# Performance work log

Hardware: AMD Instinct MI355X
Metric: run time of the kernel (lower is better)

Reference implementation:

```python
import jax, jax.numpy as jnp
import numpy as np
from jax import lax

B, T, H, E, V, S = 32, 512, 1024, 300, 32000, 50
NL2 = 4  # 2 layers * 2 directions of encoder hidden


def setup_inputs() -> dict:
    key = jax.random.key(0)
    ks = jax.random.split(key, 20)
    w = 0.05  # small init scale to keep tanh/softmax well-conditioned
    return {
        "enc_out": jax.random.normal(ks[0], (B, T, H), jnp.float32),
        "enc_h": jax.random.normal(ks[1], (NL2, B, H // 2), jnp.float32),
        "enc_c": jax.random.normal(ks[2], (NL2, B, H // 2), jnp.float32),
        "embedding": jax.random.normal(ks[3], (V, E), jnp.float32),
        "attn_W": jax.random.normal(ks[4], (H, 2 * H), jnp.float32) * w,
        "attn_b": jnp.zeros((H,), jnp.float32),
        "v": jax.random.normal(ks[5], (H,), jnp.float32) * w,
        "Wih0": jax.random.normal(ks[6], (4 * H, E + H), jnp.float32) * w,
        "Whh0": jax.random.normal(ks[7], (4 * H, H), jnp.float32) * w,
        "bih0": jnp.zeros((4 * H,), jnp.float32),
        "bhh0": jnp.zeros((4 * H,), jnp.float32),
        "Wih1": jax.random.normal(ks[8], (4 * H, H), jnp.float32) * w,
        "Whh1": jax.random.normal(ks[9], (4 * H, H), jnp.float32) * w,
        "bih1": jnp.zeros((4 * H,), jnp.float32),
        "bhh1": jnp.zeros((4 * H,), jnp.float32),
        "genW": jax.random.normal(ks[10], (V, H), jnp.float32) * w,
        "genb": jnp.zeros((V,), jnp.float32),
        "question": jax.random.randint(ks[11], (B, S), 0, V, jnp.int64),
    }


def _lstm_cell(x, h, c, Wih, Whh, bih, bhh):
    # torch gate order: i, f, g, o
    g = x @ Wih.T + bih + h @ Whh.T + bhh
    i, f, gg, o = jnp.split(g, 4, axis=-1)
    c2 = jax.nn.sigmoid(f) * c + jax.nn.sigmoid(i) * jnp.tanh(gg)
    h2 = jax.nn.sigmoid(o) * jnp.tanh(c2)
    return h2, c2


def reference(enc_out, enc_h, enc_c, embedding, attn_W, attn_b, v,
              Wih0, Whh0, bih0, bhh0, Wih1, Whh1, bih1, bhh1,
              genW, genb, question):
    # merge bidirectional encoder halves: (2L,B,H/2) -> (L,B,H)
    h0 = jnp.concatenate([enc_h[0::2], enc_h[1::2]], axis=2)
    c0 = jnp.concatenate([enc_c[0::2], enc_c[1::2]], axis=2)

    def step(carry, tok):
        h, c = carry  # each (L, B, H)
        emb = embedding[tok]  # (B, E); dropout is identity (eval mode)
        hid = h[-1]  # (B, H), last-layer hidden drives attention
        Hrep = jnp.broadcast_to(hid[:, None, :], enc_out.shape)  # (B,T,H)
        energy = jnp.tanh(jnp.concatenate([Hrep, enc_out], axis=-1) @ attn_W.T + attn_b)
        scores = jnp.einsum('bth,h->bt', energy, v)
        aw = jax.nn.softmax(scores, axis=1)  # (B, T)
        ctx = jnp.einsum('bt,bth->bh', aw, enc_out)  # (B, H)
        x = jnp.concatenate([emb, ctx], axis=-1)  # (B, E+H)
        h0n, c0n = _lstm_cell(x, h[0], c[0], Wih0, Whh0, bih0, bhh0)
        h1n, c1n = _lstm_cell(h0n, h[1], c[1], Wih1, Whh1, bih1, bhh1)
        out = jax.nn.log_softmax(h1n @ genW.T + genb, axis=-1)  # (B, V)
        return (jnp.stack([h0n, h1n]), jnp.stack([c0n, c1n])), out

    _, outs = lax.scan(step, (h0, c0), question.T)  # outs: (S, B, V)
    return jnp.transpose(outs, (1, 0, 2))  # (B, S, V)
```

## Files before the change

kernel.cpp:

```cpp
#include <hip/hip_runtime.h>
#include <hip/hip_bf16.h>
#include <math.h>

#define DEVI static __device__ __forceinline__

namespace {
constexpr int B = 32, T = 512, H = 1024, E = 300, V = 32000, S = 50;
constexpr int KX = E + H;
constexpr int K0 = 2368;
constexpr int K1 = 2048;
constexpr int MG = V + H;
}

typedef __bf16 bf16x8 __attribute__((ext_vector_type(8)));
typedef float f32x4 __attribute__((ext_vector_type(4)));

DEVI float bf2f(unsigned short u) { union { unsigned int i; float f; } v; v.i = (unsigned int)u << 16; return v.f; }
DEVI unsigned short f2bf(float f) {
  union { float f; unsigned int i; } v; v.f = f;
  unsigned int x = v.i;
  return (unsigned short)((x + 0x7fffu + ((x >> 16) & 1u)) >> 16);
}
DEVI unsigned char f2e4m3(float x) {
  union { float f; unsigned int u; } v;
  v.f = x;
  unsigned int s = (v.u >> 24) & 0x80u;
  v.u &= 0x7FFFFFFFu;
  if (v.f >= 448.0f) return (unsigned char)(s | 0x7E);
  if (v.f < 0.015625f) {
    int q = (int)rintf(v.f * 512.0f);
    return (unsigned char)(s | (unsigned int)q);
  }
  unsigned int u = v.u;
  unsigned int lsb = (u >> 20) & 1u;
  u += 0x0007FFFFu + lsb;
  unsigned int exp = (u >> 23) - 120u;
  unsigned int man = (u >> 20) & 7u;
  return (unsigned char)(s | (exp << 3) | man);
}
DEVI float e4m3f(unsigned int u) {
  unsigned int bits = ((u & 0x80u) << 24) | ((u & 0x7Fu) << 20);
  union { unsigned int i; float f; } v; v.i = bits;
  return v.f * 0x1p120f;
}
#if __has_builtin(__builtin_amdgcn_rcpf)
DEVI float frcp(float x) { return __builtin_amdgcn_rcpf(x); }
#else
DEVI float frcp(float x) { return 1.0f / x; }
#endif
DEVI float sigm(float x) { return frcp(1.0f + __expf(-x)); }
DEVI float tanh_(float x) { return 1.0f - 2.0f * frcp(__expf(2.0f * x) + 1.0f); }

__global__ __launch_bounds__(256) void k_cast_gen(const float* __restrict__ genW,
    const float* __restrict__ attn_W, unsigned char* __restrict__ Wbig8) {
  size_t i4 = ((size_t)blockIdx.x * 256 + threadIdx.x) * 4;
  if (i4 >= (size_t)MG * H) return;
  int row = (int)(i4 >> 10), k = (int)(i4 & 1023);
  const float* src = row < V ? &genW[((size_t)row << 10) + k]
                             : &attn_W[(size_t)(row - V) * (2 * H) + k];
  float4 v = *(const float4*)src;
  uchar4 o; o.x = f2e4m3(v.x); o.y = f2e4m3(v.y); o.z = f2e4m3(v.z); o.w = f2e4m3(v.w);
  *(uchar4*)&Wbig8[i4] = o;
}

__global__ __launch_bounds__(256) void k_cast_l0(const float* __restrict__ Wih,
    const float* __restrict__ Whh, unsigned short* __restrict__ Wc) {
  int m = blockIdx.x;
  int g = m & 3, n = m >> 2, srow = g * H + n;
  for (int i = threadIdx.x; i < K0 / 4; i += 256) {
    int k = i * 4;
    float4 v;
    if (k < KX) v = *(const float4*)&Wih[(size_t)srow * KX + k];
    else if (k < KX + H) v = *(const float4*)&Whh[(size_t)srow * H + (k - KX)];
    else v = make_float4(0.f, 0.f, 0.f, 0.f);
    ushort4 o; o.x = f2bf(v.x); o.y = f2bf(v.y); o.z = f2bf(v.z); o.w = f2bf(v.w);
    *(ushort4*)&Wc[(size_t)m * K0 + k] = o;
  }
}

__global__ __launch_bounds__(256) void k_cast_l1(const float* __restrict__ Wih,
    const float* __restrict__ Whh, unsigned short* __restrict__ Wc) {
  int m = blockIdx.x;
  int g = m & 3, n = m >> 2, srow = g * H + n;
  for (int i = threadIdx.x; i < K1 / 4; i += 256) {
    int k = i * 4;
    float4 v = (k < H) ? *(const float4*)&Wih[(size_t)srow * H + k]
                       : *(const float4*)&Whh[(size_t)srow * H + (k - H)];
    ushort4 o; o.x = f2bf(v.x); o.y = f2bf(v.y); o.z = f2bf(v.z); o.w = f2bf(v.w);
    *(ushort4*)&Wc[(size_t)m * K1 + k] = o;
  }
}

__global__ __launch_bounds__(256) void k_cast_attnr(const float* __restrict__ attn_W,
                                                    unsigned short* __restrict__ Wr) {
  size_t i4 = ((size_t)blockIdx.x * 256 + threadIdx.x) * 4;
  if (i4 >= (size_t)H * H) return;
  int n = (int)(i4 >> 10), k = (int)(i4 & 1023);
  float4 v = *(const float4*)&attn_W[(size_t)n * (2 * H) + H + k];
  ushort4 o; o.x = f2bf(v.x); o.y = f2bf(v.y); o.z = f2bf(v.z); o.w = f2bf(v.w);
  *(ushort4*)&Wr[i4] = o;
}

__global__ void k_bias(const float* bih0, const float* bhh0,
                       const float* bih1, const float* bhh1,
                       float* bc0, float* bc1) {
  int idx = blockIdx.x * 256 + threadIdx.x;
  if (idx < 4096) { int g = idx & 3, n = idx >> 2; bc0[idx] = bih0[g * H + n] + bhh0[g * H + n]; }
  else if (idx < 8192) { int m = idx - 4096; int g = m & 3, n = m >> 2; bc1[m] = bih1[g * H + n] + bhh1[g * H + n]; }
}

__global__ __launch_bounds__(256) void k_cast_enc(const float* __restrict__ src,
    unsigned short* __restrict__ dst, unsigned char* __restrict__ dst8) {
  size_t i4 = ((size_t)blockIdx.x * 256 + threadIdx.x) * 4;
  if (i4 >= (size_t)B * T * H) return;
  float4 v = *(const float4*)&src[i4];
  ushort4 o; o.x = f2bf(v.x); o.y = f2bf(v.y); o.z = f2bf(v.z); o.w = f2bf(v.w);
  *(ushort4*)&dst[i4] = o;
  uchar4 o8; o8.x = f2e4m3(v.x); o8.y = f2e4m3(v.y); o8.z = f2e4m3(v.z); o8.w = f2e4m3(v.w);
  *(uchar4*)&dst8[i4] = o8;
}

__global__ __launch_bounds__(256) void k_init(const float* __restrict__ enc_h,
    const float* __restrict__ enc_c, float* __restrict__ cbuf,
    unsigned short* __restrict__ xc0_0, unsigned short* __restrict__ xc0_1,
    unsigned short* __restrict__ xc1_0, unsigned char* __restrict__ hgen8) {
  int idx = blockIdx.x * 256 + threadIdx.x;
  if (idx < 2 * B * H) {
    int l = idx >> 15, r = idx & 32767, b = r >> 10, hh = r & 1023;
    int half = hh >> 9, hr = hh & 511;
    int src = (2 * l + half) * B * (H / 2) + b * (H / 2) + hr;
    cbuf[idx] = enc_c[src];
    float hv = enc_h[src];
    if (l == 0) xc0_0[(size_t)b * K0 + KX + hh] = f2bf(hv);
    else { xc1_0[(size_t)b * K1 + H + hh] = f2bf(hv); hgen8[(size_t)b * H + hh] = f2e4m3(hv); }
  } else if (idx < 2 * B * H + 2 * B * 20) {
    int j = idx - 2 * B * H;
    int p = j / (B * 20), rr = j % (B * 20), b = rr / 20, kk = rr % 20;
    (p ? xc0_1 : xc0_0)[(size_t)b * K0 + KX + H + kk] = 0;
  }
}

__global__ __launch_bounds__(256) void k_encproj_mfma(const unsigned short* __restrict__ Wr,
    const unsigned short* __restrict__ Xb, const float* __restrict__ attn_b,
    unsigned char* __restrict__ encp8) {
  int wv = threadIdx.x >> 6, lane = threadIdx.x & 63;
  int n0w = blockIdx.x * 64 + wv * 16;
  int m0 = blockIdx.y * 64;
  const unsigned short* Wp = Wr + (size_t)(n0w + (lane & 15)) * H + (lane >> 4) * 8;
  const unsigned short* Xp = Xb + (size_t)(m0 + (lane & 15)) * H + (lane >> 4) * 8;
  f32x4 acc[4] = {{0.f,0.f,0.f,0.f},{0.f,0.f,0.f,0.f},{0.f,0.f,0.f,0.f},{0.f,0.f,0.f,0.f}};
#pragma unroll 2
  for (int k0 = 0; k0 < H; k0 += 32) {
    bf16x8 a = *(const bf16x8*)(Wp + k0);
#pragma unroll
    for (int g = 0; g < 4; g++) {
      bf16x8 b = *(const bf16x8*)(Xp + (size_t)g * 16 * H + k0);
      acc[g] = __builtin_amdgcn_mfma_f32_16x16x32_bf16(a, b, acc[g], 0, 0, 0);
    }
  }
  int nb = n0w + (lane >> 4) * 4;
  f32x4 bi = *(const f32x4*)&attn_b[nb];
#pragma unroll
  for (int g = 0; g < 4; g++) {
    int m = m0 + g * 16 + (lane & 15);
    f32x4 o = acc[g] + bi;
    uchar4 ob; ob.x = f2e4m3(o[0]); ob.y = f2e4m3(o[1]); ob.z = f2e4m3(o[2]); ob.w = f2e4m3(o[3]);
    *(uchar4*)&encp8[(size_t)m * H + nb] = ob;
  }
}

DEVI void gemm_tile_fp8(const unsigned char* __restrict__ W, const unsigned char* __restrict__ X,
                        int m0w, int lane, f32x4& acc0, f32x4& acc1) {
  const unsigned char* Wp = W + (size_t)(m0w + (lane & 15)) * 1024 + (lane >> 4) * 8;
  const unsigned char* Xp = X + (size_t)(lane & 15) * 1024 + (lane >> 4) * 8;
#pragma unroll 4
  for (int k0 = 0; k0 < 1024; k0 += 32) {
    long a  = *(const long*)(Wp + k0);
    long b0 = *(const long*)(Xp + k0);
    long b1 = *(const long*)(Xp + 16 * 1024 + k0);
    acc0 = __builtin_amdgcn_mfma_f32_16x16x32_fp8_fp8(a, b0, acc0, 0, 0, 0);
    acc1 = __builtin_amdgcn_mfma_f32_16x16x32_fp8_fp8(a, b1, acc1, 0, 0, 0);
  }
}

__global__ __launch_bounds__(256, 4) void k_gemm_out_fp8(const unsigned char* __restrict__ W,
    const unsigned char* __restrict__ X, const float* __restrict__ bias, int M0,
    float* __restrict__ out0, int ld0, float* __restrict__ out1, int ld1,
    float* __restrict__ part) {
  __shared__ float esum[4][32];
  int wv = threadIdx.x >> 6, lane = threadIdx.x & 63;
  int m0w = blockIdx.x * 64 + wv * 16;
  f32x4 acc0 = {0.f, 0.f, 0.f, 0.f}, acc1 = acc0;
  gemm_tile_fp8(W, X, m0w, lane, acc0, acc1);
  int r0 = m0w + (lane >> 4) * 4;
  int b = lane & 15;
  float s0 = 0.f, s1 = 0.f;
  if (r0 < M0) {
    f32x4 bi = *(const f32x4*)&bias[r0];
    f32x4 o0 = acc0 + bi, o1 = acc1 + bi;
    *(f32x4*)&out0[(size_t)b * ld0 + r0] = o0;
    *(f32x4*)&out0[(size_t)(b + 16) * ld0 + r0] = o1;
    s0 = __expf(o0[0]) + __expf(o0[1]) + __expf(o0[2]) + __expf(o0[3]);
    s1 = __expf(o1[0]) + __expf(o1[1]) + __expf(o1[2]) + __expf(o1[3]);
  } else {
    int r = r0 - M0;
    *(f32x4*)&out1[(size_t)b * ld1 + r] = acc0;
    *(f32x4*)&out1[(size_t)(b + 16) * ld1 + r] = acc1;
  }
  if (part != nullptr && blockIdx.x < V / 64) {
    s0 += __shfl_xor(s0, 16, 64); s0 += __shfl_xor(s0, 32, 64);
    s1 += __shfl_xor(s1, 16, 64); s1 += __shfl_xor(s1, 32, 64);
    if (lane < 16) { esum[wv][lane] = s0; esum[wv][lane + 16] = s1; }
    __syncthreads();
    if (threadIdx.x < 32)
      part[blockIdx.x * 32 + threadIdx.x] =
          esum[0][threadIdx.x] + esum[1][threadIdx.x] + esum[2][threadIdx.x] + esum[3][threadIdx.x];
  }
}

template <int K>
__global__ __launch_bounds__(512, 2) void k_gemm_lstm(const unsigned short* __restrict__ W,
    const unsigned short* __restrict__ X, const float* __restrict__ bcomb,
    float* __restrict__ c,
    unsigned short* __restrict__ hA, int ldA_, int offA,
    unsigned short* __restrict__ hB, int ldB_, int offB,
    unsigned char* __restrict__ h8) {
  __shared__ f32x4 red[8][64][2];
  int wv = threadIdx.x >> 6, lane = threadIdx.x & 63;
  int m0w = blockIdx.x * 16;
  const unsigned short* Wp = W + (size_t)(m0w + (lane & 15)) * K + (lane >> 4) * 8;
  const unsigned short* Xp = X + (size_t)(lane & 15) * K + (lane >> 4) * 8;
  f32x4 acc0 = {0.f, 0.f, 0.f, 0.f}, acc1 = acc0;
#pragma unroll 2
  for (int k0 = wv * 32; k0 < K; k0 += 256) {
    bf16x8 a  = *(const bf16x8*)(Wp + k0);
    bf16x8 b0 = *(const bf16x8*)(Xp + k0);
    bf16x8 b1 = *(const bf16x8*)(Xp + 16 * K + k0);
    acc0 = __builtin_amdgcn_mfma_f32_16x16x32_bf16(a, b0, acc0, 0, 0, 0);
    acc1 = __builtin_amdgcn_mfma_f32_16x16x32_bf16(a, b1, acc1, 0, 0, 0);
  }
  red[wv][lane][0] = acc0;
  red[wv][lane][1] = acc1;
  __syncthreads();
  if (wv == 0) {
    acc0 = red[0][lane][0] + red[1][lane][0] + red[2][lane][0] + red[3][lane][0]
         + red[4][lane][0] + red[5][lane][0] + red[6][lane][0] + red[7][lane][0];
    acc1 = red[0][lane][1] + red[1][lane][1] + red[2][lane][1] + red[3][lane][1]
         + red[4][lane][1] + red[5][lane][1] + red[6][lane][1] + red[7][lane][1];
    int r0 = m0w + (lane >> 4) * 4;
    int n = r0 >> 2;
    f32x4 bi = *(const f32x4*)&bcomb[r0];
#pragma unroll
    for (int f = 0; f < 2; f++) {
      f32x4 g = f ? acc1 : acc0;
      int b = (lane & 15) + f * 16;
      float gi = g[0] + bi[0], gf = g[1] + bi[1];
      float gg = g[2] + bi[2], go = g[3] + bi[3];
      float cp = c[(size_t)b * H + n];
      float c2 = sigm(gf) * cp + sigm(gi) * tanh_(gg);
      c[(size_t)b * H + n] = c2;
      float h2 = sigm(go) * tanh_(c2);
      unsigned short hb = f2bf(h2);
      hA[(size_t)b * ldA_ + offA + n] = hb;
      if (hB) hB[(size_t)b * ldB_ + offB + n] = hb;
      if (h8) h8[(size_t)b * H + n] = f2e4m3(h2);
    }
  }
}

__global__ __launch_bounds__(256, 4) void k_p1(const unsigned char* __restrict__ encp8,
    const float* __restrict__ hidproj, const float* __restrict__ vvec,
    float* __restrict__ scores,
    const float* __restrict__ logits, const float* __restrict__ part,
    float* __restrict__ out,
    const float* __restrict__ embedding, const int* __restrict__ question,
    unsigned short* __restrict__ xc, int s) {
  int bx = blockIdx.x, tid = threadIdx.x;
  if (bx < 512) {
    int wv = tid >> 6, lane = tid & 63;
    int wid0 = bx * 32 + wv * 8;
    int b = wid0 >> 9;
    const float* hp = hidproj + (size_t)b * H + lane * 16;
    const float* vp = vvec + lane * 16;
    float4 h4[4], v4[4];
#pragma unroll
    for (int i = 0; i < 4; i++) { h4[i] = *(const float4*)&hp[i * 4]; v4[i] = *(const float4*)&vp[i * 4]; }
#pragma unroll
    for (int j = 0; j < 8; j++) {
      const unsigned char* ep = encp8 + (size_t)(wid0 + j) * H + lane * 16;
      uint4 u = *(const uint4*)ep;
      float acc = 0.f;
      unsigned int ws[4] = {u.x, u.y, u.z, u.w};
#pragma unroll
      for (int i = 0; i < 4; i++) {
        unsigned int wd = ws[i];
        acc += v4[i].x * tanh_(e4m3f(wd & 0xFF) + h4[i].x);
        acc += v4[i].y * tanh_(e4m3f((wd >> 8) & 0xFF) + h4[i].y);
        acc += v4[i].z * tanh_(e4m3f((wd >> 16) & 0xFF) + h4[i].z);
        acc += v4[i].w * tanh_(e4m3f(wd >> 24) + h4[i].w);
      }
#pragma unroll
      for (int off = 32; off; off >>= 1) acc += __shfl_xor(acc, off, 64);
      if (lane == 0) scores[wid0 + j] = acc;
    }
  } else if (bx < 768) {
    if (s == 0) return;
    __shared__ float red[256];
    int idx = bx - 512;
    int b = idx >> 3, ch = idx & 7;
    float ssum = 0.f;
    for (int i = tid; i < V / 64; i += 256) ssum += part[i * 32 + b];
    red[tid] = ssum; __syncthreads();
    for (int st = 128; st; st >>= 1) { if (tid < st) red[tid] += red[tid + st]; __syncthreads(); }
    float lse = __logf(red[0]);
    const float* L = logits + (size_t)b * V + ch * 4000;
    float* O = out + ((size_t)b * S + (s - 1)) * V + ch * 4000;
    for (int i = tid; i < 1000; i += 256) {
      float4 v = ((const float4*)L)[i];
      ((float4*)O)[i] = make_float4(v.x - lse, v.y - lse, v.z - lse, v.w - lse);
    }
  } else {
    int b = bx - 768;
    int tok = question[b * S + s];
    for (int e = tid; e < E; e += 256)
      xc[(size_t)b * K0 + e] = f2bf(embedding[(size_t)tok * E + e]);
  }
}

__global__ __launch_bounds__(256, 4) void k_ctx(const float* __restrict__ scores,
    const unsigned char* __restrict__ enc8, unsigned short* __restrict__ xc) {
  int b = blockIdx.x, y = blockIdx.y, tid = threadIdx.x;
  __shared__ float aw[T];
  __shared__ float red[256];
  float s0 = scores[b * T + tid], s1 = scores[b * T + 256 + tid];
  float m = fmaxf(s0, s1);
  red[tid] = m; __syncthreads();
  for (int st = 128; st; st >>= 1) { if (tid < st) red[tid] = fmaxf(red[tid], red[tid + st]); __syncthreads(); }
  m = red[0]; __syncthreads();
  float e0 = __expf(s0 - m), e1 = __expf(s1 - m);
  aw[tid] = e0; aw[tid + 256] = e1;
  red[tid] = e0 + e1; __syncthreads();
  for (int st = 128; st; st >>= 1) { if (tid < st) red[tid] += red[tid + st]; __syncthreads(); }
  float inv = frcp(red[0]);
  __syncthreads();
  int wv = tid >> 6, l = tid & 63;
  int q = l & 7, tp = l >> 3;
  const unsigned char* eb = enc8 + (size_t)b * T * H + y * 64 + q * 8;
  float a[8] = {};
  for (int it = 0; it < 16; it++) {
    int t = it * 32 + wv * 8 + tp;
    uint2 u = *(const uint2*)&eb[(size_t)t * H];
    float w = aw[t];
    a[0] += w * e4m3f(u.x & 0xFF);
    a[1] += w * e4m3f((u.x >> 8) & 0xFF);
    a[2] += w * e4m3f((u.x >> 16) & 0xFF);
    a[3] += w * e4m3f(u.x >> 24);
    a[4] += w * e4m3f(u.y & 0xFF);
    a[5] += w * e4m3f((u.y >> 8) & 0xFF);
    a[6] += w * e4m3f((u.y >> 16) & 0xFF);
    a[7] += w * e4m3f(u.y >> 24);
  }
#pragma unroll
  for (int j = 0; j < 8; j++) {
    a[j] += __shfl_xor(a[j], 8, 64);
    a[j] += __shfl_xor(a[j], 16, 64);
    a[j] += __shfl_xor(a[j], 32, 64);
  }
  __syncthreads();
  if (tp == 0) {
#pragma unroll
    for (int j = 0; j < 8; j++) red[wv * 64 + q * 8 + j] = a[j];
  }
  __syncthreads();
  if (tid < 64) {
    float val = (red[tid] + red[64 + tid] + red[128 + tid] + red[192 + tid]) * inv;
    xc[(size_t)b * K0 + E + y * 64 + tid] = f2bf(val);
  }
}

__global__ __launch_bounds__(256) void k_lsB(const float* __restrict__ logits,
    const float* __restrict__ part, float* __restrict__ out, int s) {
  int b = blockIdx.x, ch = blockIdx.y, tid = threadIdx.x;
  __shared__ float red[256];
  float ssum = 0.f;
  for (int i = tid; i < V / 64; i += 256) ssum += part[i * 32 + b];
  red[tid] = ssum; __syncthreads();
  for (int st = 128; st; st >>= 1) { if (tid < st) red[tid] += red[tid + st]; __syncthreads(); }
  float lse = __logf(red[0]);
  const float* L = logits + (size_t)b * V + ch * 4000;
  float* O = out + ((size_t)b * S + s) * V + ch * 4000;
  for (int i = tid; i < 1000; i += 256) {
    float4 v = ((const float4*)L)[i];
    ((float4*)O)[i] = make_float4(v.x - lse, v.y - lse, v.z - lse, v.w - lse);
  }
}

extern "C" void kernel_launch(void* const* d_in, const int* in_sizes, int n_in,
                              void* d_out, int out_size, void* d_ws, size_t ws_size,
                              hipStream_t stream) {
  const float* enc_out   = (const float*)d_in[0];
  const float* enc_h     = (const float*)d_in[1];
  const float* enc_c     = (const float*)d_in[2];
  const float* embedding = (const float*)d_in[3];
  const float* attn_W    = (const float*)d_in[4];
  const float* attn_b    = (const float*)d_in[5];
  const float* vvec      = (const float*)d_in[6];
  const float* Wih0      = (const float*)d_in[7];
  const float* Whh0      = (const float*)d_in[8];
  const float* bih0      = (const float*)d_in[9];
  const float* bhh0      = (const float*)d_in[10];
  const float* Wih1      = (const float*)d_in[11];
  const float* Whh1      = (const float*)d_in[12];
  const float* bih1      = (const float*)d_in[13];
  const float* bhh1      = (const float*)d_in[14];
  const float* genW      = (const float*)d_in[15];
  const float* genb      = (const float*)d_in[16];
  const int*   question  = (const int*)d_in[17];
  float* out = (float*)d_out;

  char* w = (char*)d_ws;
  auto alloc = [&](size_t bytes) { char* r = w; w += (bytes + 255) & ~(size_t)255; return r; };
  unsigned char*  Wbig8 = (unsigned char*)alloc((size_t)MG * H);
  unsigned short* Wc0   = (unsigned short*)alloc((size_t)4096 * K0 * 2);
  unsigned short* Wc1   = (unsigned short*)alloc((size_t)4096 * K1 * 2);
  unsigned short* encb  = (unsigned short*)alloc((size_t)B * T * H * 2);
  unsigned char*  encb8 = (unsigned char*)alloc((size_t)B * T * H);
  unsigned char*  encp8 = (unsigned char*)alloc((size_t)B * T * H);
  unsigned short* Wr    = (unsigned short*)alloc((size_t)H * H * 2);
  float* bcomb0 = (float*)alloc(4096 * 4);
  float* bcomb1 = (float*)alloc(4096 * 4);
  float* cbuf   = (float*)alloc((size_t)2 * B * H * 4);
  unsigned short* xc0[2] = {(unsigned short*)alloc((size_t)B * K0 * 2),
                            (unsigned short*)alloc((size_t)B * K0 * 2)};
  unsigned short* xc1[2] = {(unsigned short*)alloc((size_t)B * K1 * 2),
                            (unsigned short*)alloc((size_t)B * K1 * 2)};
  unsigned char*  hgen8 = (unsigned char*)alloc((size_t)B * H);
  float* hidproj = (float*)alloc((size_t)B * H * 4);
  float* scores  = (float*)alloc((size_t)B * T * 4);
  float* logits  = (float*)alloc((size_t)B * V * 4);
  float* part    = (float*)alloc((size_t)(V / 64) * 32 * 4);

  k_cast_gen<<<(int)(((size_t)MG * H / 4 + 255) / 256), 256, 0, stream>>>(genW, attn_W, Wbig8);
  k_cast_l0<<<4096, 256, 0, stream>>>(Wih0, Whh0, Wc0);
  k_cast_l1<<<4096, 256, 0, stream>>>(Wih1, Whh1, Wc1);
  k_cast_attnr<<<H * H / 4 / 256, 256, 0, stream>>>(attn_W, Wr);
  k_bias<<<32, 256, 0, stream>>>(bih0, bhh0, bih1, bhh1, bcomb0, bcomb1);
  k_cast_enc<<<(B * T * H / 4) / 256, 256, 0, stream>>>(enc_out, encb, encb8);
  k_init<<<(2 * B * H + 2 * B * 20 + 255) / 256, 256, 0, stream>>>(
      enc_h, enc_c, cbuf, xc0[0], xc0[1], xc1[0], hgen8);
  k_encproj_mfma<<<dim3(H / 64, B * T / 64), 256, 0, stream>>>(Wr, encb, attn_b, encp8);
  k_gemm_out_fp8<<<H / 64, 256, 0, stream>>>(
      Wbig8 + (size_t)V * H, hgen8, nullptr, 0, nullptr, 0, hidproj, H, nullptr);

  for (int s = 0; s < S; s++) {
    int par = s & 1;
    k_p1<<<800, 256, 0, stream>>>(encp8, hidproj, vvec, scores,
                                  logits, part, out, embedding, question, xc0[par], s);
    k_ctx<<<dim3(B, 16), 256, 0, stream>>>(scores, encb8, xc0[par]);
    k_gemm_lstm<K0><<<4096 / 16, 512, 0, stream>>>(
        Wc0, xc0[par], bcomb0, cbuf,
        xc0[par ^ 1], K0, KX,
        xc1[par], K1, 0,
        nullptr);
    k_gemm_lstm<K1><<<4096 / 16, 512, 0, stream>>>(
        Wc1, xc1[par], bcomb1, cbuf + B * H,
        xc1[par ^ 1], K1, H,
        nullptr, 0, 0,
        hgen8);
    k_gemm_out_fp8<<<MG / 64, 256, 0, stream>>>(
        Wbig8, hgen8, genb, V, logits, V, hidproj, H, part);
  }
  k_lsB<<<dim3(B, 8), 256, 0, stream>>>(logits, part, out, S - 1);
}
```

Measured before the change: 3.870 ms.

## Pipeline vocab GEMM into context kernel and fuse hidden projection via spin counter

```diff
diff --git a/kernel.cpp b/kernel.cpp
--- a/kernel.cpp
+++ b/kernel.cpp
@@ -224,9 +224,24 @@
     float* __restrict__ c,
     unsigned short* __restrict__ hA, int ldA_, int offA,
     unsigned short* __restrict__ hB, int ldB_, int offB,
-    unsigned char* __restrict__ h8) {
+    unsigned char* __restrict__ h8,
+    const unsigned char* __restrict__ WL, float* __restrict__ hidproj,
+    int* __restrict__ ctr, int target) {
+  int tid = threadIdx.x;
+  int wv = tid >> 6, lane = tid & 63;
+  if (WL != nullptr && blockIdx.x >= 256) {
+    if (tid == 0) { while (atomicAdd(ctr, 0) < target) { } }
+    __syncthreads();
+    __threadfence();
+    int m0w = (blockIdx.x - 256) * 128 + wv * 16;
+    f32x4 a0 = {0.f, 0.f, 0.f, 0.f}, a1 = a0;
+    gemm_tile_fp8(WL, h8, m0w, lane, a0, a1);
+    int r0 = m0w + (lane >> 4) * 4, b = lane & 15;
+    *(f32x4*)&hidproj[(size_t)b * H + r0] = a0;
+    *(f32x4*)&hidproj[(size_t)(b + 16) * H + r0] = a1;
+    return;
+  }
   __shared__ f32x4 red[8][64][2];
-  int wv = threadIdx.x >> 6, lane = threadIdx.x & 63;
   int m0w = blockIdx.x * 16;
   const unsigned short* Wp = W + (size_t)(m0w + (lane & 15)) * K + (lane >> 4) * 8;
   const unsigned short* Xp = X + (size_t)(lane & 15) * K + (lane >> 4) * 8;
@@ -266,12 +281,16 @@
       if (h8) h8[(size_t)b * H + n] = f2e4m3(h2);
     }
   }
+  if (ctr != nullptr) {
+    __syncthreads();
+    if (tid == 0) { __threadfence(); atomicAdd(ctr, 1); }
+  }
 }
 
 __global__ __launch_bounds__(256, 4) void k_p1(const unsigned char* __restrict__ encp8,
     const float* __restrict__ hidproj, const float* __restrict__ vvec,
     float* __restrict__ scores,
-    const float* __restrict__ logits, const float* __restrict__ part,
+    const float* __restrict__ logitsR, const float* __restrict__ partR,
     float* __restrict__ out,
     const float* __restrict__ embedding, const int* __restrict__ question,
     unsigned short* __restrict__ xc, int s) {
@@ -304,17 +323,17 @@
       if (lane == 0) scores[wid0 + j] = acc;
     }
   } else if (bx < 768) {
-    if (s == 0) return;
+    if (s < 2) return;
     __shared__ float red[256];
     int idx = bx - 512;
     int b = idx >> 3, ch = idx & 7;
     float ssum = 0.f;
-    for (int i = tid; i < V / 64; i += 256) ssum += part[i * 32 + b];
+    for (int i = tid; i < V / 64; i += 256) ssum += partR[i * 32 + b];
     red[tid] = ssum; __syncthreads();
     for (int st = 128; st; st >>= 1) { if (tid < st) red[tid] += red[tid + st]; __syncthreads(); }
     float lse = __logf(red[0]);
-    const float* L = logits + (size_t)b * V + ch * 4000;
-    float* O = out + ((size_t)b * S + (s - 1)) * V + ch * 4000;
+    const float* L = logitsR + (size_t)b * V + ch * 4000;
+    float* O = out + ((size_t)b * S + (s - 2)) * V + ch * 4000;
     for (int i = tid; i < 1000; i += 256) {
       float4 v = ((const float4*)L)[i];
       ((float4*)O)[i] = make_float4(v.x - lse, v.y - lse, v.z - lse, v.w - lse);
@@ -327,11 +346,40 @@
   }
 }
 
-__global__ __launch_bounds__(256, 4) void k_ctx(const float* __restrict__ scores,
-    const unsigned char* __restrict__ enc8, unsigned short* __restrict__ xc) {
-  int b = blockIdx.x, y = blockIdx.y, tid = threadIdx.x;
+__global__ __launch_bounds__(256, 4) void k2(const float* __restrict__ scores,
+    const unsigned char* __restrict__ enc8, unsigned short* __restrict__ xc,
+    const unsigned char* __restrict__ Wbig8, const unsigned char* __restrict__ hgen8,
+    const float* __restrict__ genb,
+    float* __restrict__ logitsW, float* __restrict__ partW, int s) {
+  int bx = blockIdx.x, tid = threadIdx.x;
   __shared__ float aw[T];
   __shared__ float red[256];
+  __shared__ float esum[4][32];
+  if (bx < 1000 && (bx & 1)) {
+    if (s == 0) return;
+    int task = bx >> 1;
+    int wv = tid >> 6, lane = tid & 63;
+    int m0w = task * 64 + wv * 16;
+    f32x4 a0 = {0.f, 0.f, 0.f, 0.f}, a1 = a0;
+    gemm_tile_fp8(Wbig8, hgen8, m0w, lane, a0, a1);
+    int r0 = m0w + (lane >> 4) * 4;
+    int b = lane & 15;
+    f32x4 bi = *(const f32x4*)&genb[r0];
+    f32x4 o0 = a0 + bi, o1 = a1 + bi;
+    *(f32x4*)&logitsW[(size_t)b * V + r0] = o0;
+    *(f32x4*)&logitsW[(size_t)(b + 16) * V + r0] = o1;
+    float s0 = __expf(o0[0]) + __expf(o0[1]) + __expf(o0[2]) + __expf(o0[3]);
+    float s1 = __expf(o1[0]) + __expf(o1[1]) + __expf(o1[2]) + __expf(o1[3]);
+    s0 += __shfl_xor(s0, 16, 64); s0 += __shfl_xor(s0, 32, 64);
+    s1 += __shfl_xor(s1, 16, 64); s1 += __shfl_xor(s1, 32, 64);
+    if (lane < 16) { esum[wv][lane] = s0; esum[wv][lane + 16] = s1; }
+    __syncthreads();
+    if (tid < 32)
+      partW[task * 32 + tid] = esum[0][tid] + esum[1][tid] + esum[2][tid] + esum[3][tid];
+    return;
+  }
+  int c = (bx < 1000) ? (bx >> 1) : (500 + (bx - 1000));
+  int b = c >> 4, y = c & 15;
   float s0 = scores[b * T + tid], s1 = scores[b * T + 256 + tid];
   float m = fmaxf(s0, s1);
   red[tid] = m; __syncthreads();
@@ -437,9 +485,11 @@
   unsigned char*  hgen8 = (unsigned char*)alloc((size_t)B * H);
   float* hidproj = (float*)alloc((size_t)B * H * 4);
   float* scores  = (float*)alloc((size_t)B * T * 4);
-  float* logits  = (float*)alloc((size_t)B * V * 4);
-  float* part    = (float*)alloc((size_t)(V / 64) * 32 * 4);
-
+  float* logits[2] = {(float*)alloc((size_t)B * V * 4), (float*)alloc((size_t)B * V * 4)};
+  float* part[2]   = {(float*)alloc((size_t)(V / 64) * 32 * 4), (float*)alloc((size_t)(V / 64) * 32 * 4)};
+  int* ctr = (int*)alloc(256);
+
+  hipMemsetAsync(ctr, 0, 4, stream);
   k_cast_gen<<<(int)(((size_t)MG * H / 4 + 255) / 256), 256, 0, stream>>>(genW, attn_W, Wbig8);
   k_cast_l0<<<4096, 256, 0, stream>>>(Wih0, Whh0, Wc0);
   k_cast_l1<<<4096, 256, 0, stream>>>(Wih1, Whh1, Wc1);
@@ -455,20 +505,26 @@
   for (int s = 0; s < S; s++) {
     int par = s & 1;
     k_p1<<<800, 256, 0, stream>>>(encp8, hidproj, vvec, scores,
-                                  logits, part, out, embedding, question, xc0[par], s);
-    k_ctx<<<dim3(B, 16), 256, 0, stream>>>(scores, encb8, xc0[par]);
-    k_gemm_lstm<K0><<<4096 / 16, 512, 0, stream>>>(
+                                  logits[par], part[par],
+                                  out, embedding, question, xc0[par], s);
+    k2<<<1012, 256, 0, stream>>>(scores, encb8, xc0[par],
+                                 Wbig8, hgen8, genb,
+                                 logits[par ^ 1], part[par ^ 1], s);
+    k_gemm_lstm<K0><<<256, 512, 0, stream>>>(
         Wc0, xc0[par], bcomb0, cbuf,
         xc0[par ^ 1], K0, KX,
         xc1[par], K1, 0,
-        nullptr);
-    k_gemm_lstm<K1><<<4096 / 16, 512, 0, stream>>>(
+        nullptr,
+        nullptr, nullptr, nullptr, 0);
+    k_gemm_lstm<K1><<<264, 512, 0, stream>>>(
         Wc1, xc1[par], bcomb1, cbuf + B * H,
         xc1[par ^ 1], K1, H,
         nullptr, 0, 0,
-        hgen8);
-    k_gemm_out_fp8<<<MG / 64, 256, 0, stream>>>(
-        Wbig8, hgen8, genb, V, logits, V, hidproj, H, part);
-  }
-  k_lsB<<<dim3(B, 8), 256, 0, stream>>>(logits, part, out, S - 1);
-}
+        hgen8,
+        Wbig8 + (size_t)V * H, hidproj, ctr, 256 * (s + 1));
+  }
+  k_gemm_out_fp8<<<V / 64, 256, 0, stream>>>(
+      Wbig8, hgen8, genb, V, logits[(S - 1) & 1], V, nullptr, 0, part[(S - 1) & 1]);
+  k_lsB<<<dim3(B, 8), 256, 0, stream>>>(logits[(S - 2) & 1], part[(S - 2) & 1], out, S - 2);
+  k_lsB<<<dim3(B, 8), 256, 0, stream>>>(logits[(S - 1) & 1], part[(S - 1) & 1], out, S - 1);
+}
```

After: 5.610 ms. 1.45x slower.
